# Optimization experiments

Measured on AMD Instinct MI355X. Metric: run time of the kernel, lower is better.

Reference implementation:

```python
import jax, jax.numpy as jnp
import numpy as np

N_CELLS = 100000
N_ISO = 16
K_PLUS_1 = 31  # self + 30 neighbors, per sklearn kneighbors convention


def setup_inputs() -> dict:
    key = jax.random.key(0)
    k1, k2, k3, k4, k5 = jax.random.split(key, 5)
    return {
        "unsplice": jax.random.normal(k1, (N_CELLS,), dtype=jnp.float32),
        "splices": jax.random.normal(k2, (N_CELLS, N_ISO), dtype=jnp.float32),
        "unsplice_predict": jax.random.normal(k3, (N_CELLS,), dtype=jnp.float32),
        "splice_predicts": jax.random.normal(k4, (N_CELLS, N_ISO), dtype=jnp.float32),
        "indices": jax.random.randint(k5, (N_CELLS, K_PLUS_1), 0, N_CELLS, dtype=jnp.int64),
    }


def reference(unsplice, splices, unsplice_predict, splice_predicts, indices):
    # Velocity vector per cell in (1 + n_isoforms)-dim space: v = (du, ds_1..ds_K)
    uv = unsplice_predict - unsplice                      # [N]
    sv = splice_predicts - splices                        # [N, I]
    v = jnp.concatenate([uv[:, None], sv], axis=1)        # [N, D], D = I+1

    nbr = indices[:, 1:]                                  # [N, K] drop self
    # Neighbor displacement vectors vn[i,k] = x[nbr[i,k]] - x[i]
    un = unsplice[nbr] - unsplice[:, None]                # [N, K]
    sn = splices[nbr] - splices[:, None, :]               # [N, K, I]
    vn = jnp.concatenate([un[..., None], sn], axis=-1)    # [N, K, D]

    dots = jnp.einsum('nd,nkd->nk', v, vn)                # [N, K]
    vi_norm = jnp.linalg.norm(v, axis=1)                  # [N]
    vn_norm = jnp.linalg.norm(vn, axis=2)                 # [N, K]
    denom = vi_norm[:, None] * vn_norm
    denom = jnp.where(denom == 0, jnp.ones_like(denom), denom)
    cos_sim = dots / denom                                # [N, K]
    cost = 1.0 - jnp.max(cos_sim, axis=1)                 # [N]
    return jnp.mean(cost)
```

## Files before the change

### kernel.cpp

```cpp
#include <hip/hip_runtime.h>
#include <math.h>

#define N_CELLS_C 100000
#define N_ISO_C 16
#define KP1_C 31
#define BLOCK 256
#define CPB 64

__device__ __forceinline__ int idx_shift(const char* idx_bytes) {
    const int lane = threadIdx.x & 63;
    int probe = 0;
    if (lane < 16) probe = ((const int*)idx_bytes)[2 * lane + 1];
    return __any(probe != 0) ? 2 : 3;
}

__device__ __forceinline__ unsigned enc14(float x) {
    const _Float16 h = (_Float16)x;
    const unsigned short b = __builtin_bit_cast(unsigned short, h);
    return (((unsigned)b + 2u) >> 2) & 0x3FFFu;
}
__device__ __forceinline__ float dec14(unsigned v) {
    const unsigned short b = (unsigned short)(v << 2);
    const _Float16 h = __builtin_bit_cast(_Float16, b);
    return (float)h;
}

__global__ __launch_bounds__(BLOCK) void pack_kernel(
    const float* __restrict__ unsplice,
    const float* __restrict__ splices,
    unsigned* __restrict__ rec)
{
    const int cell = blockIdx.x * BLOCK + threadIdx.x;
    if (cell >= N_CELLS_C) return;
    const float4* row = (const float4*)(splices + (long long)cell * N_ISO_C);
    const float4 r0 = row[0], r1 = row[1], r2 = row[2], r3 = row[3];
    float vals[17] = { r0.x, r0.y, r0.z, r0.w, r1.x, r1.y, r1.z, r1.w,
                       r2.x, r2.y, r2.z, r2.w, r3.x, r3.y, r3.z, r3.w,
                       unsplice[cell] };
    unsigned w[8] = {0, 0, 0, 0, 0, 0, 0, 0};
    #pragma unroll
    for (int i = 0; i < 17; ++i) {
        const unsigned v = enc14(vals[i]);
        const int s = 14 * i, k = s >> 5, off = s & 31;
        w[k] |= v << off;
        if (off > 18) w[k + 1] |= v >> (32 - off);
    }
    uint4* dst = (uint4*)(rec + (size_t)cell * 8);
    dst[0] = uint4{w[0], w[1], w[2], w[3]};
    dst[1] = uint4{w[4], w[5], w[6], w[7]};
}

__global__ __launch_bounds__(BLOCK) void cost_kernel(
    const float* __restrict__ unsplice,
    const float* __restrict__ splices,
    const float* __restrict__ unsplice_predict,
    const float* __restrict__ splice_predicts,
    const char*  __restrict__ idx_bytes,
    const unsigned* __restrict__ rec,
    float*       __restrict__ partials)
{
    const int tid  = threadIdx.x;
    const int q    = tid & 3;
    const int cell = blockIdx.x * CPB + (tid >> 2);
    const int shift = idx_shift(idx_bytes);

    float cost = 0.0f;
    if (cell < N_CELLS_C) {
        float ci[17], v[17];
        {
            const float4* sr = (const float4*)(splices         + (long long)cell * N_ISO_C);
            const float4* pr = (const float4*)(splice_predicts + (long long)cell * N_ISO_C);
            #pragma unroll
            for (int b = 0; b < 4; ++b) {
                const float4 s4 = sr[b], p4 = pr[b];
                ci[4*b+0] = s4.x; ci[4*b+1] = s4.y; ci[4*b+2] = s4.z; ci[4*b+3] = s4.w;
                v[4*b+0] = p4.x - s4.x; v[4*b+1] = p4.y - s4.y;
                v[4*b+2] = p4.z - s4.z; v[4*b+3] = p4.w - s4.w;
            }
            ci[16] = unsplice[cell];
            v[16]  = unsplice_predict[cell] - ci[16];
        }
        float vn2 = 0.f;
        #pragma unroll
        for (int i = 0; i < 17; ++i) vn2 = fmaf(v[i], v[i], vn2);
        const float inv_vi = (vn2 > 0.f) ? rsqrtf(vn2) : 0.f;

        const long long base = (long long)cell * KP1_C;
        int jv[8];
        #pragma unroll
        for (int t = 0; t < 8; ++t) {
            int k = 1 + q + 4 * t;
            if (k > 30) k = 30;
            jv[t] = *(const int*)(idx_bytes + ((base + k) << shift));
        }

        float maxq = -INFINITY;
        #pragma unroll
        for (int c2 = 0; c2 < 2; ++c2) {
            uint4 ga[4], gb[4];
            #pragma unroll
            for (int t = 0; t < 4; ++t) {
                const uint4* p = (const uint4*)(rec + (size_t)jv[c2 * 4 + t] * 8);
                ga[t] = p[0];
                gb[t] = p[1];
            }
            #pragma unroll
            for (int t = 0; t < 4; ++t) {
                const unsigned w[8] = { ga[t].x, ga[t].y, ga[t].z, ga[t].w,
                                        gb[t].x, gb[t].y, gb[t].z, gb[t].w };
                float dot = 0.f, nn2 = 0.f;
                #pragma unroll
                for (int i = 0; i < 17; ++i) {
                    const int s = 14 * i, k = s >> 5, off = s & 31;
                    unsigned raw = w[k] >> off;
                    if (off > 18) raw |= w[k + 1] << (32 - off);
                    const float g = dec14(raw & 0x3FFFu);
                    const float d = g - ci[i];
                    dot = fmaf(v[i], d, dot);
                    nn2 = fmaf(d, d, nn2);
                }
                const float rn = (nn2 > 0.f) ? rsqrtf(nn2) : 0.f;
                maxq = fmaxf(maxq, dot * rn);
            }
        }
        maxq = fmaxf(maxq, __shfl_xor(maxq, 1));
        maxq = fmaxf(maxq, __shfl_xor(maxq, 2));
        if (q == 0) cost = 1.0f - maxq * inv_vi;
    }

    for (int off = 32; off > 0; off >>= 1) cost += __shfl_down(cost, off);
    __shared__ float wsum[BLOCK / 64];
    if ((tid & 63) == 0) wsum[tid >> 6] = cost;
    __syncthreads();
    if (tid == 0) {
        float s = 0.f;
        #pragma unroll
        for (int wv = 0; wv < BLOCK / 64; ++wv) s += wsum[wv];
        partials[blockIdx.x] = s;
    }
}

__global__ __launch_bounds__(BLOCK) void cost_kernel_f32(
    const float* __restrict__ unsplice,
    const float* __restrict__ splices,
    const float* __restrict__ unsplice_predict,
    const float* __restrict__ splice_predicts,
    const char*  __restrict__ idx_bytes,
    float*       __restrict__ partials)
{
    const int tid  = threadIdx.x;
    const int q    = tid & 3;
    const int cell = blockIdx.x * (BLOCK / 4) + (tid >> 2);
    const int shift = idx_shift(idx_bytes);

    float cost = 0.0f;
    if (cell < N_CELLS_C) {
        const float u_i = unsplice[cell];
        const float uv  = unsplice_predict[cell] - u_i;
        const float4 s4  = *(const float4*)(splices         + (long long)cell * N_ISO_C + 4 * q);
        const float4 sp4 = *(const float4*)(splice_predicts + (long long)cell * N_ISO_C + 4 * q);
        const float v0 = sp4.x - s4.x, v1 = sp4.y - s4.y, v2 = sp4.z - s4.z, v3 = sp4.w - s4.w;
        float vpp = v0*v0 + v1*v1 + v2*v2 + v3*v3;
        vpp += __shfl_xor(vpp, 1);
        vpp += __shfl_xor(vpp, 2);
        const float vn2 = vpp + uv * uv;
        const float inv_vi = (vn2 > 0.0f) ? rsqrtf(vn2) : 0.0f;
        const long long base = (long long)cell * KP1_C;
        float maxq = -INFINITY;
        #pragma unroll
        for (int k = 1; k < KP1_C; ++k) {
            const int j = *(const int*)(idx_bytes + ((base + k) << shift));
            const float unj = unsplice[j];
            const float4 n4 = *(const float4*)(splices + (long long)j * N_ISO_C + 4 * q);
            const float d0 = n4.x - s4.x, d1 = n4.y - s4.y, d2 = n4.z - s4.z, d3 = n4.w - s4.w;
            float dp = v0*d0 + v1*d1 + v2*d2 + v3*d3;
            float np = d0*d0 + d1*d1 + d2*d2 + d3*d3;
            dp += __shfl_xor(dp, 1);  np += __shfl_xor(np, 1);
            dp += __shfl_xor(dp, 2);  np += __shfl_xor(np, 2);
            const float un  = unj - u_i;
            const float dot = dp + uv * un;
            const float nn2 = np + un * un;
            const float rn  = (nn2 > 0.0f) ? rsqrtf(nn2) : 0.0f;
            maxq = fmaxf(maxq, dot * rn);
        }
        if (q == 0) cost = 1.0f - maxq * inv_vi;
    }
    for (int off = 32; off > 0; off >>= 1) cost += __shfl_down(cost, off);
    __shared__ float wsum[BLOCK / 64];
    if ((tid & 63) == 0) wsum[tid >> 6] = cost;
    __syncthreads();
    if (tid == 0) {
        float s = 0.0f;
        #pragma unroll
        for (int wv = 0; wv < BLOCK / 64; ++wv) s += wsum[wv];
        partials[blockIdx.x] = s;
    }
}

__global__ __launch_bounds__(BLOCK) void final_reduce_kernel(
    const float* __restrict__ partials, int nparts, float* __restrict__ out)
{
    float s = 0.0f;
    for (int i = threadIdx.x; i < nparts; i += BLOCK) s += partials[i];
    for (int off = 32; off > 0; off >>= 1) s += __shfl_down(s, off);
    __shared__ float wsum[BLOCK / 64];
    if ((threadIdx.x & 63) == 0) wsum[threadIdx.x >> 6] = s;
    __syncthreads();
    if (threadIdx.x == 0) {
        float t = 0.0f;
        #pragma unroll
        for (int wv = 0; wv < BLOCK / 64; ++wv) t += wsum[wv];
        out[0] = t / (float)N_CELLS_C;
    }
}

extern "C" void kernel_launch(void* const* d_in, const int* in_sizes, int n_in,
                              void* d_out, int out_size, void* d_ws, size_t ws_size,
                              hipStream_t stream) {
    const float* unsplice         = (const float*)d_in[0];
    const float* splices          = (const float*)d_in[1];
    const float* unsplice_predict = (const float*)d_in[2];
    const float* splice_predicts  = (const float*)d_in[3];
    const char*  idx_bytes        = (const char*)d_in[4];
    float* out = (float*)d_out;

    unsigned* rec      = (unsigned*)d_ws;
    float*    partials = (float*)((char*)d_ws + 3200000);

    const size_t req = 3200000 + 8 * 4096;

    if (ws_size >= req) {
        const int pack_blocks = (N_CELLS_C + BLOCK - 1) / BLOCK;
        pack_kernel<<<pack_blocks, BLOCK, 0, stream>>>(unsplice, splices, rec);
        const int nblocks = (N_CELLS_C + CPB - 1) / CPB;
        cost_kernel<<<nblocks, BLOCK, 0, stream>>>(
            unsplice, splices, unsplice_predict, splice_predicts,
            idx_bytes, rec, partials);
        final_reduce_kernel<<<1, BLOCK, 0, stream>>>(partials, nblocks, out);
    } else {
        float* fb_partials = (float*)d_ws;
        const int nblocks = (N_CELLS_C + (BLOCK / 4) - 1) / (BLOCK / 4);
        cost_kernel_f32<<<nblocks, BLOCK, 0, stream>>>(
            unsplice, splices, unsplice_predict, splice_predicts,
            idx_bytes, fb_partials);
        final_reduce_kernel<<<1, BLOCK, 0, stream>>>(fb_partials, nblocks, out);
    }
}
```

Baseline: 41.15 us.

## Split each neighbor record across two lanes with 9-element halves

```diff
diff --git a/kernel.cpp b/kernel.cpp
--- a/kernel.cpp
+++ b/kernel.cpp
@@ -5,7 +5,6 @@
 #define N_ISO_C 16
 #define KP1_C 31
 #define BLOCK 256
-#define CPB 64
 
 __device__ __forceinline__ int idx_shift(const char* idx_bytes) {
     const int lane = threadIdx.x & 63;
@@ -34,23 +33,29 @@
     if (cell >= N_CELLS_C) return;
     const float4* row = (const float4*)(splices + (long long)cell * N_ISO_C);
     const float4 r0 = row[0], r1 = row[1], r2 = row[2], r3 = row[3];
-    float vals[17] = { r0.x, r0.y, r0.z, r0.w, r1.x, r1.y, r1.z, r1.w,
-                       r2.x, r2.y, r2.z, r2.w, r3.x, r3.y, r3.z, r3.w,
-                       unsplice[cell] };
-    unsigned w[8] = {0, 0, 0, 0, 0, 0, 0, 0};
-    #pragma unroll
-    for (int i = 0; i < 17; ++i) {
-        const unsigned v = enc14(vals[i]);
+    const float h0[9] = { r0.x, r0.y, r0.z, r0.w, r1.x, r1.y, r1.z, r1.w, r2.x };
+    const float h1[8] = { r2.y, r2.z, r2.w, r3.x, r3.y, r3.z, r3.w, unsplice[cell] };
+    unsigned w[8] = {0,0,0,0,0,0,0,0};
+    #pragma unroll
+    for (int i = 0; i < 9; ++i) {
+        const unsigned v = enc14(h0[i]);
         const int s = 14 * i, k = s >> 5, off = s & 31;
         w[k] |= v << off;
         if (off > 18) w[k + 1] |= v >> (32 - off);
     }
+    #pragma unroll
+    for (int i = 0; i < 8; ++i) {
+        const unsigned v = enc14(h1[i]);
+        const int s = 14 * i, k = 4 + (s >> 5), off = s & 31;
+        w[k] |= v << off;
+        if (off > 18) w[k + 1] |= v >> (32 - off);
+    }
     uint4* dst = (uint4*)(rec + (size_t)cell * 8);
     dst[0] = uint4{w[0], w[1], w[2], w[3]};
     dst[1] = uint4{w[4], w[5], w[6], w[7]};
 }
 
-__global__ __launch_bounds__(BLOCK) void cost_kernel(
+__global__ __launch_bounds__(BLOCK, 8) void cost_kernel(
     const float* __restrict__ unsplice,
     const float* __restrict__ splices,
     const float* __restrict__ unsplice_predict,
@@ -60,73 +65,79 @@
     float*       __restrict__ partials)
 {
     const int tid  = threadIdx.x;
-    const int q    = tid & 3;
-    const int cell = blockIdx.x * CPB + (tid >> 2);
+    const int sub  = tid & 7;
+    const int w    = sub & 1;
+    const int p    = sub >> 1;
+    const int cell = blockIdx.x * (BLOCK / 8) + (tid >> 3);
     const int shift = idx_shift(idx_bytes);
 
-    float cost = 0.0f;
-    if (cell < N_CELLS_C) {
-        float ci[17], v[17];
-        {
-            const float4* sr = (const float4*)(splices         + (long long)cell * N_ISO_C);
-            const float4* pr = (const float4*)(splice_predicts + (long long)cell * N_ISO_C);
+    float ci[9], v[9];
+    {
+        const float4* sr = (const float4*)(splices         + (long long)cell * N_ISO_C);
+        const float4* pr = (const float4*)(splice_predicts + (long long)cell * N_ISO_C);
+        if (w == 0) {
+            const float4 a = sr[0], b = sr[1]; const float c2 = sr[2].x;
+            const float4 pa = pr[0], pb = pr[1]; const float pc2 = pr[2].x;
+            ci[0]=a.x; ci[1]=a.y; ci[2]=a.z; ci[3]=a.w;
+            ci[4]=b.x; ci[5]=b.y; ci[6]=b.z; ci[7]=b.w; ci[8]=c2;
+            v[0]=pa.x-a.x; v[1]=pa.y-a.y; v[2]=pa.z-a.z; v[3]=pa.w-a.w;
+            v[4]=pb.x-b.x; v[5]=pb.y-b.y; v[6]=pb.z-b.z; v[7]=pb.w-b.w; v[8]=pc2-c2;
+        } else {
+            const float4 a = sr[2], b = sr[3];
+            const float4 pa = pr[2], pb = pr[3];
+            const float u  = unsplice[cell], up = unsplice_predict[cell];
+            ci[0]=a.y; ci[1]=a.z; ci[2]=a.w;
+            ci[3]=b.x; ci[4]=b.y; ci[5]=b.z; ci[6]=b.w; ci[7]=u; ci[8]=0.f;
+            v[0]=pa.y-a.y; v[1]=pa.z-a.z; v[2]=pa.w-a.w;
+            v[3]=pb.x-b.x; v[4]=pb.y-b.y; v[5]=pb.z-b.z; v[6]=pb.w-b.w;
+            v[7]=up-u; v[8]=0.f;
+        }
+    }
+    float vp = 0.f;
+    #pragma unroll
+    for (int i = 0; i < 9; ++i) vp = fmaf(v[i], v[i], vp);
+    vp += __shfl_xor(vp, 1);
+    const float inv_vi = (vp > 0.f) ? rsqrtf(vp) : 0.f;
+
+    const long long base = (long long)cell * KP1_C;
+    int jv[8];
+    #pragma unroll
+    for (int t = 0; t < 8; ++t) {
+        int k = 1 + p + 4 * t;
+        if (k > 30) k = 30;
+        jv[t] = *(const int*)(idx_bytes + ((base + k) << shift));
+    }
+
+    float maxq = -INFINITY;
+    #pragma unroll
+    for (int c2 = 0; c2 < 2; ++c2) {
+        uint4 G[4];
+        #pragma unroll
+        for (int t = 0; t < 4; ++t)
+            G[t] = *(const uint4*)(rec + (size_t)jv[c2 * 4 + t] * 8 + 4 * w);
+        #pragma unroll
+        for (int t = 0; t < 4; ++t) {
+            const unsigned wd[4] = { G[t].x, G[t].y, G[t].z, G[t].w };
+            float dp = 0.f, np = 0.f;
             #pragma unroll
-            for (int b = 0; b < 4; ++b) {
-                const float4 s4 = sr[b], p4 = pr[b];
-                ci[4*b+0] = s4.x; ci[4*b+1] = s4.y; ci[4*b+2] = s4.z; ci[4*b+3] = s4.w;
-                v[4*b+0] = p4.x - s4.x; v[4*b+1] = p4.y - s4.y;
-                v[4*b+2] = p4.z - s4.z; v[4*b+3] = p4.w - s4.w;
+            for (int i = 0; i < 9; ++i) {
+                const int s = 14 * i, k = s >> 5, off = s & 31;
+                unsigned raw = wd[k] >> off;
+                if (off > 18) raw |= wd[k + 1] << (32 - off);
+                const float g = dec14(raw & 0x3FFFu);
+                const float d = g - ci[i];
+                dp = fmaf(v[i], d, dp);
+                np = fmaf(d, d, np);
             }
-            ci[16] = unsplice[cell];
-            v[16]  = unsplice_predict[cell] - ci[16];
+            dp += __shfl_xor(dp, 1);
+            np += __shfl_xor(np, 1);
+            const float rn = (np > 0.f) ? rsqrtf(np) : 0.f;
+            maxq = fmaxf(maxq, dp * rn);
         }
-        float vn2 = 0.f;
-        #pragma unroll
-        for (int i = 0; i < 17; ++i) vn2 = fmaf(v[i], v[i], vn2);
-        const float inv_vi = (vn2 > 0.f) ? rsqrtf(vn2) : 0.f;
-
-        const long long base = (long long)cell * KP1_C;
-        int jv[8];
-        #pragma unroll
-        for (int t = 0; t < 8; ++t) {
-            int k = 1 + q + 4 * t;
-            if (k > 30) k = 30;
-            jv[t] = *(const int*)(idx_bytes + ((base + k) << shift));
-        }
-
-        float maxq = -INFINITY;
-        #pragma unroll
-        for (int c2 = 0; c2 < 2; ++c2) {
-            uint4 ga[4], gb[4];
-            #pragma unroll
-            for (int t = 0; t < 4; ++t) {
-                const uint4* p = (const uint4*)(rec + (size_t)jv[c2 * 4 + t] * 8);
-                ga[t] = p[0];
-                gb[t] = p[1];
-            }
-            #pragma unroll
-            for (int t = 0; t < 4; ++t) {
-                const unsigned w[8] = { ga[t].x, ga[t].y, ga[t].z, ga[t].w,
-                                        gb[t].x, gb[t].y, gb[t].z, gb[t].w };
-                float dot = 0.f, nn2 = 0.f;
-                #pragma unroll
-                for (int i = 0; i < 17; ++i) {
-                    const int s = 14 * i, k = s >> 5, off = s & 31;
-                    unsigned raw = w[k] >> off;
-                    if (off > 18) raw |= w[k + 1] << (32 - off);
-                    const float g = dec14(raw & 0x3FFFu);
-                    const float d = g - ci[i];
-                    dot = fmaf(v[i], d, dot);
-                    nn2 = fmaf(d, d, nn2);
-                }
-                const float rn = (nn2 > 0.f) ? rsqrtf(nn2) : 0.f;
-                maxq = fmaxf(maxq, dot * rn);
-            }
-        }
-        maxq = fmaxf(maxq, __shfl_xor(maxq, 1));
-        maxq = fmaxf(maxq, __shfl_xor(maxq, 2));
-        if (q == 0) cost = 1.0f - maxq * inv_vi;
-    }
+    }
+    maxq = fmaxf(maxq, __shfl_xor(maxq, 2));
+    maxq = fmaxf(maxq, __shfl_xor(maxq, 4));
+    float cost = (sub == 0) ? (1.0f - maxq * inv_vi) : 0.f;
 
     for (int off = 32; off > 0; off >>= 1) cost += __shfl_down(cost, off);
     __shared__ float wsum[BLOCK / 64];
@@ -227,12 +238,12 @@
     unsigned* rec      = (unsigned*)d_ws;
     float*    partials = (float*)((char*)d_ws + 3200000);
 
-    const size_t req = 3200000 + 8 * 4096;
+    const size_t req = 3200000 + 16 * 4096;
 
     if (ws_size >= req) {
         const int pack_blocks = (N_CELLS_C + BLOCK - 1) / BLOCK;
         pack_kernel<<<pack_blocks, BLOCK, 0, stream>>>(unsplice, splices, rec);
-        const int nblocks = (N_CELLS_C + CPB - 1) / CPB;
+        const int nblocks = N_CELLS_C / (BLOCK / 8);
         cost_kernel<<<nblocks, BLOCK, 0, stream>>>(
             unsplice, splices, unsplice_predict, splice_predicts,
             idx_bytes, rec, partials);
```

New measurement: 39.14 us. 1.05x faster.
